# Performance work log

Hardware: AMD Instinct MI355X
Metric: run time of the kernel (lower is better)

## Reference

```python
import jax, jax.numpy as jnp
import numpy as np

B, S, H, I = 4, 2048, 2048, 5504


def setup_inputs() -> dict:
    key = jax.random.key(0)
    k1, k2, k3, k4 = jax.random.split(key, 4)
    scale = 0.02
    return {
        "hidden_state": jax.random.normal(k1, (B, S, H), dtype=jnp.float32),
        "w_gate": jax.random.normal(k2, (I, H), dtype=jnp.float32) * scale,  # gate_proj.weight [out,in]
        "w_up": jax.random.normal(k3, (I, H), dtype=jnp.float32) * scale,    # up_proj.weight
        "w_down": jax.random.normal(k4, (H, I), dtype=jnp.float32) * scale,  # down_proj.weight
    }


def reference(hidden_state, w_gate, w_up, w_down):
    # SwiGLU: act(x W_g^T) * (x W_u^T)
    gate = jax.nn.silu(jnp.einsum("bsh,ih->bsi", hidden_state, w_gate))
    up = jnp.einsum("bsh,ih->bsi", hidden_state, w_up)
    intermediate = gate * up  # [B,S,I]

    # Neuron impacts. Original broadcasts (B,I,1)*(1,I,H) and sums over H;
    # algebraically identical to s[b,i] * ||w_up[i,:]||^2, which we use to
    # avoid materializing the [B,I,H] tensor. Same math, same result.
    s = jnp.sum(intermediate ** 2, axis=1)          # sum over seq dim -> [B,I]
    row_sq = jnp.sum(w_up ** 2, axis=-1)            # [I]
    impacts = jnp.sqrt(s * row_sq[None, :])          # [B,I]

    out = jnp.einsum("bsi,hi->bsh", intermediate, w_down)  # down_proj
    return out, impacts
```

## Files before the change

kernel.cpp:

```cpp
#include <hip/hip_runtime.h>
#include <stdint.h>
#include <stddef.h>

typedef __attribute__((ext_vector_type(8))) short short8;
typedef __attribute__((ext_vector_type(4))) float f32x4;
typedef unsigned short u16;

#define B_ 4
#define S_ 2048
#define H_ 2048
#define I_ 5504
#define M_ 8192

__device__ __forceinline__ u16 f2bf(float f) {
  uint32_t u = __float_as_uint(f);
  u += 0x7fff + ((u >> 16) & 1);
  return (u16)(u >> 16);
}

#define GLOAD_LDS16(src, dst)                                                            \
  __builtin_amdgcn_global_load_lds((const __attribute__((address_space(1))) void*)(src), \
                                   (__attribute__((address_space(3))) void*)(dst), 16, 0, 0)

__global__ __launch_bounds__(256) void cvt_f32_bf16(const float* __restrict__ in,
                                                    u16* __restrict__ out, int n4) {
  int i = blockIdx.x * 256 + threadIdx.x;
  if (i < n4) {
    float4 v = ((const float4*)in)[i];
    ushort4 o;
    o.x = f2bf(v.x); o.y = f2bf(v.y); o.z = f2bf(v.z); o.w = f2bf(v.w);
    ((ushort4*)out)[i] = o;
  }
}

__global__ __launch_bounds__(256) void cvt_wcat(const float* __restrict__ wg,
                                                const float* __restrict__ wu,
                                                u16* __restrict__ wcat) {
  const int i = blockIdx.x * 256 + threadIdx.x;
  const int f = i * 4;
  const int r = f >> 11;
  const int c = f & 2047;
  const int srcrow = (r >> 5) * 16 + (r & 15);
  const float* src = (((r >> 4) & 1) ? wu : wg) + (size_t)srcrow * 2048 + c;
  float4 v = *(const float4*)src;
  ushort4 o;
  o.x = f2bf(v.x); o.y = f2bf(v.y); o.z = f2bf(v.z); o.w = f2bf(v.w);
  *(ushort4*)(wcat + (size_t)r * 2048 + c) = o;
}

#define WAITLGK0 asm volatile("s_waitcnt lgkmcnt(0)" ::: "memory")
#define PH_BAR asm volatile("s_barrier" ::: "memory")

#define MM2(av, bx, by, N0, N1)                                                             \
  {                                                                                         \
    __builtin_amdgcn_s_setprio(1);                                                          \
    _Pragma("unroll") for (int m = 0; m < 8; ++m) {                                         \
      acc[m][N0] = __builtin_amdgcn_mfma_f32_16x16x32_bf16(av[m], bx, acc[m][N0], 0, 0, 0); \
      acc[m][N1] = __builtin_amdgcn_mfma_f32_16x16x32_bf16(av[m], by, acc[m][N1], 0, 0, 0); \
    }                                                                                       \
    __builtin_amdgcn_s_setprio(0);                                                          \
  }

template <int EPI>
__global__ __launch_bounds__(512, 1) void gemm8(const u16* __restrict__ A,
                                                const u16* __restrict__ Bm, const int K,
                                                const int NT, float* __restrict__ outf,
                                                u16* __restrict__ inter, float* __restrict__ s) {
  __shared__ __align__(16) char lds_raw[131072 + 512];

  const int nwg = gridDim.x;
  const int cpx = nwg >> 3;
  const int swz = (blockIdx.x & 7) * cpx + (blockIdx.x >> 3);
  const int mt = swz / NT;
  const int nt = swz % NT;

  const int tid = threadIdx.x;
  const int lane = tid & 63;
  const int wid = tid >> 6;
  const int wr = wid >> 2;
  const int wc = wid & 3;
  const int l15 = lane & 15;

  if (tid < 128) ((float*)(lds_raw + 131072))[tid] = 0.f;

  const int chunkx = (l15 >> 1) & 3;
  const int aoff = (wr * 128 + l15) * 64 + (((lane >> 4) ^ chunkx) << 4);
  const int boff = (wc * 64 + l15) * 64 + (((lane >> 4) ^ chunkx) << 4);

  const u16* Abase = A + (size_t)(mt * 256) * K;
  const u16* Bbase = Bm + (size_t)(nt * 256) * K;

  int goff[2], loff[2];
#pragma unroll
  for (int i = 0; i < 2; ++i) {
    const int f = tid * 16 + i * 8192;
    const int row = f >> 6;
    const int cl = (f >> 4) & 3;
    goff[i] = row * K + 8 * (cl ^ ((row >> 1) & 3));
    loff[i] = (tid >> 6) * 1024 + i * 8192;
  }

#define STG(v, q)                                                              \
  {                                                                            \
    const u16* _b = ((q) < 2 ? Abase : Bbase) + (v) * 64 + ((q) & 1) * 32;     \
    char* _s = lds_raw + (((v) & 1) * 65536 + (q) * 16384);                    \
    GLOAD_LDS16(_b + goff[0], _s + loff[0]);                                   \
    GLOAD_LDS16(_b + goff[1], _s + loff[1]);                                   \
  }
#define RDA8(dst, c, ks)                                 \
  _Pragma("unroll") for (int m = 0; m < 8; ++m) dst[m] = \
      *(const short8*)(lds_raw + (c) * 65536 + (ks) * 16384 + aoff + m * 1024);
#define RDB(dst, c, ks, n) \
  dst = *(const short8*)(lds_raw + (c) * 65536 + 32768 + (ks) * 16384 + boff + (n) * 1024);

  f32x4 acc[8][4] = {};
  short8 a[8], a2[8];

  const int T = K >> 6;

  STG(0, 0); STG(0, 1); STG(0, 2); STG(0, 3);
  STG(1, 0); STG(1, 2); STG(1, 1);
  asm volatile("s_waitcnt vmcnt(6)" ::: "memory");
  PH_BAR;

#pragma unroll 1
  for (int t = 0; t < T; ++t) {
    const int c = t & 1;
    const bool s1 = (t + 1 < T);
    const bool s2 = (t + 2 < T);
    short8 b0x, b0y, b1x, b1y, b2x, b2y, b3x, b3y;
    RDA8(a, c, 0);
    RDB(b0x, c, 0, 0);
    RDB(b0y, c, 0, 1);
    if (s1) STG(t + 1, 3);
    WAITLGK0;
    PH_BAR;
    MM2(a, b0x, b0y, 0, 1);
    RDB(b1x, c, 0, 2);
    RDB(b1y, c, 0, 3);
    if (s2) STG(t + 2, 0);
    WAITLGK0;
    PH_BAR;
    MM2(a, b1x, b1y, 2, 3);
    RDA8(a2, c, 1);
    RDB(b2x, c, 1, 0);
    RDB(b2y, c, 1, 1);
    if (s2) STG(t + 2, 2);
    WAITLGK0;
    PH_BAR;
    MM2(a2, b2x, b2y, 0, 1);
    RDB(b3x, c, 1, 2);
    RDB(b3y, c, 1, 3);
    if (s2) STG(t + 2, 1);
    if (s2) {
      asm volatile("s_waitcnt vmcnt(6) lgkmcnt(0)" ::: "memory");
    } else {
      asm volatile("s_waitcnt vmcnt(0) lgkmcnt(0)" ::: "memory");
    }
    PH_BAR;
    MM2(a2, b3x, b3y, 2, 3);
  }

  const int r0 = mt * 256 + wr * 128 + (lane >> 4) * 4;
  if constexpr (EPI == 0) {
    const int c0 = nt * 256 + wc * 64 + l15;
#pragma unroll
    for (int m = 0; m < 8; ++m)
#pragma unroll
      for (int n = 0; n < 4; ++n)
#pragma unroll
        for (int j = 0; j < 4; ++j)
          outf[(size_t)(r0 + m * 16 + j) * 2048 + (c0 + n * 16)] = acc[m][n][j];
  } else {
    float* s_tile = (float*)(lds_raw + 131072);
    const int c0 = nt * 128 + wc * 32 + l15;
    float sp0 = 0.f, sp1 = 0.f;
#pragma unroll
    for (int m = 0; m < 8; ++m) {
#pragma unroll
      for (int j = 0; j < 4; ++j) {
        {
          const float g = acc[m][0][j], u = acc[m][1][j];
          const float v = (g / (1.f + __expf(-g))) * u;
          sp0 += v * v;
          inter[(size_t)(r0 + m * 16 + j) * I_ + c0] = f2bf(v);
        }
        {
          const float g = acc[m][2][j], u = acc[m][3][j];
          const float v = (g / (1.f + __expf(-g))) * u;
          sp1 += v * v;
          inter[(size_t)(r0 + m * 16 + j) * I_ + (c0 + 16)] = f2bf(v);
        }
      }
    }
    atomicAdd(&s_tile[wc * 32 + l15], sp0);
    atomicAdd(&s_tile[wc * 32 + 16 + l15], sp1);
    __syncthreads();
    if (tid < 128) atomicAdd(&s[(mt >> 3) * I_ + nt * 128 + tid], s_tile[tid]);
  }
#undef STG
#undef RDA8
#undef RDB
}

__global__ __launch_bounds__(256) void rowsq_impacts(const float* __restrict__ wu,
                                                     const float* __restrict__ s,
                                                     float* __restrict__ imp) {
  const int i = blockIdx.x;
  const int tid = threadIdx.x;
  const float4* row = (const float4*)(wu + (size_t)i * H_);
  float acc = 0.f;
#pragma unroll
  for (int t = 0; t < 2; ++t) {
    float4 v = row[tid + t * 256];
    acc += v.x * v.x + v.y * v.y + v.z * v.z + v.w * v.w;
  }
#pragma unroll
  for (int off = 32; off > 0; off >>= 1) acc += __shfl_down(acc, off, 64);
  __shared__ float wsum[4];
  if ((tid & 63) == 0) wsum[tid >> 6] = acc;
  __syncthreads();
  if (tid == 0) {
    const float rs = wsum[0] + wsum[1] + wsum[2] + wsum[3];
#pragma unroll
    for (int b = 0; b < 4; ++b) imp[b * I_ + i] = sqrtf(s[b * I_ + i] * rs);
  }
}

extern "C" void kernel_launch(void* const* d_in, const int* in_sizes, int n_in,
                              void* d_out, int out_size, void* d_ws, size_t ws_size,
                              hipStream_t stream) {
  const float* x = (const float*)d_in[0];
  const float* wg = (const float*)d_in[1];
  const float* wu = (const float*)d_in[2];
  const float* wd = (const float*)d_in[3];
  float* out = (float*)d_out;
  float* imp = out + (size_t)M_ * H_;

  char* ws = (char*)d_ws;
  u16* xb = (u16*)(ws);
  u16* wcatb = (u16*)(ws + 33554432);
  u16* wdb = (u16*)(ws + 78643200);
  u16* interb = (u16*)(ws + 101187584);
  float* s = (float*)(ws + 191365120);

  cvt_f32_bf16<<<16384, 256, 0, stream>>>(x, xb, (M_ * H_) / 4);
  cvt_wcat<<<22016, 256, 0, stream>>>(wg, wu, wcatb);
  cvt_f32_bf16<<<11008, 256, 0, stream>>>(wd, wdb, (H_ * I_) / 4);
  hipMemsetAsync(s, 0, (size_t)B_ * I_ * sizeof(float), stream);

  gemm8<1><<<1376, 512, 0, stream>>>(xb, wcatb, 2048, 43, nullptr, interb, s);
  gemm8<0><<<256, 512, 0, stream>>>(interb, wdb, 5504, 8, out, nullptr, nullptr);
  rowsq_impacts<<<I_, 256, 0, stream>>>(wu, s, imp);
}
```

Measured before the change: 713.2 us.

## Restructure GEMM main loop into quadrant-based MFMA phases with reused fragments

```diff
diff --git a/kernel.cpp b/kernel.cpp
--- a/kernel.cpp
+++ b/kernel.cpp
@@ -51,14 +51,16 @@
 #define WAITLGK0 asm volatile("s_waitcnt lgkmcnt(0)" ::: "memory")
 #define PH_BAR asm volatile("s_barrier" ::: "memory")
 
-#define MM2(av, bx, by, N0, N1)                                                             \
-  {                                                                                         \
-    __builtin_amdgcn_s_setprio(1);                                                          \
-    _Pragma("unroll") for (int m = 0; m < 8; ++m) {                                         \
-      acc[m][N0] = __builtin_amdgcn_mfma_f32_16x16x32_bf16(av[m], bx, acc[m][N0], 0, 0, 0); \
-      acc[m][N1] = __builtin_amdgcn_mfma_f32_16x16x32_bf16(av[m], by, acc[m][N1], 0, 0, 0); \
-    }                                                                                       \
-    __builtin_amdgcn_s_setprio(0);                                                          \
+#define MMQ(AF, BF, MB, N0)                                                              \
+  {                                                                                      \
+    __builtin_amdgcn_s_setprio(1);                                                       \
+    _Pragma("unroll") for (int m = 0; m < 4; ++m) _Pragma("unroll") for (int n = 0; n < 2; ++n) { \
+      acc[MB + m][N0 + n] =                                                              \
+          __builtin_amdgcn_mfma_f32_16x16x32_bf16(AF[0][m], BF[0][n], acc[MB + m][N0 + n], 0, 0, 0); \
+      acc[MB + m][N0 + n] =                                                              \
+          __builtin_amdgcn_mfma_f32_16x16x32_bf16(AF[1][m], BF[1][n], acc[MB + m][N0 + n], 0, 0, 0); \
+    }                                                                                    \
+    __builtin_amdgcn_s_setprio(0);                                                       \
   }
 
 template <int EPI>
@@ -100,27 +102,29 @@
     loff[i] = (tid >> 6) * 1024 + i * 8192;
   }
 
-#define STG(v, q)                                                              \
-  {                                                                            \
-    const u16* _b = ((q) < 2 ? Abase : Bbase) + (v) * 64 + ((q) & 1) * 32;     \
-    char* _s = lds_raw + (((v) & 1) * 65536 + (q) * 16384);                    \
-    GLOAD_LDS16(_b + goff[0], _s + loff[0]);                                   \
-    GLOAD_LDS16(_b + goff[1], _s + loff[1]);                                   \
-  }
-#define RDA8(dst, c, ks)                                 \
-  _Pragma("unroll") for (int m = 0; m < 8; ++m) dst[m] = \
-      *(const short8*)(lds_raw + (c) * 65536 + (ks) * 16384 + aoff + m * 1024);
-#define RDB(dst, c, ks, n) \
-  dst = *(const short8*)(lds_raw + (c) * 65536 + 32768 + (ks) * 16384 + boff + (n) * 1024);
+#define STG(v, q)                                                          \
+  {                                                                        \
+    const u16* _b = ((q) < 2 ? Abase : Bbase) + (v) * 64 + ((q) & 1) * 32; \
+    char* _s = lds_raw + (((v) & 1) * 65536 + (q) * 16384);                \
+    GLOAD_LDS16(_b + goff[0], _s + loff[0]);                               \
+    GLOAD_LDS16(_b + goff[1], _s + loff[1]);                               \
+  }
+#define RDAQ(dst, c, MB)                                                              \
+  _Pragma("unroll") for (int ks = 0; ks < 2; ++ks) _Pragma("unroll") for (int m = 0; m < 4; ++m) \
+      dst[ks][m] = *(const short8*)(lds_raw + (c) * 65536 + ks * 16384 + aoff + (MB + m) * 1024);
+#define RDBQ(dst, c, NB)                                                              \
+  _Pragma("unroll") for (int ks = 0; ks < 2; ++ks) _Pragma("unroll") for (int n = 0; n < 2; ++n) \
+      dst[ks][n] =                                                                    \
+          *(const short8*)(lds_raw + (c) * 65536 + 32768 + ks * 16384 + boff + (NB + n) * 1024);
 
   f32x4 acc[8][4] = {};
-  short8 a[8], a2[8];
+  short8 alo[2][4], ahi[2][4], b01[2][2], b23[2][2];
 
   const int T = K >> 6;
 
   STG(0, 0); STG(0, 1); STG(0, 2); STG(0, 3);
-  STG(1, 0); STG(1, 2); STG(1, 1);
-  asm volatile("s_waitcnt vmcnt(6)" ::: "memory");
+  STG(1, 2); STG(1, 3);
+  asm volatile("s_waitcnt vmcnt(4)" ::: "memory");
   PH_BAR;
 
 #pragma unroll 1
@@ -128,37 +132,34 @@
     const int c = t & 1;
     const bool s1 = (t + 1 < T);
     const bool s2 = (t + 2 < T);
-    short8 b0x, b0y, b1x, b1y, b2x, b2y, b3x, b3y;
-    RDA8(a, c, 0);
-    RDB(b0x, c, 0, 0);
-    RDB(b0y, c, 0, 1);
-    if (s1) STG(t + 1, 3);
+    RDAQ(alo, c, 0);
+    RDBQ(b01, c, 0);
+    if (s1) STG(t + 1, 0);
+    PH_BAR;
     WAITLGK0;
-    PH_BAR;
-    MM2(a, b0x, b0y, 0, 1);
-    RDB(b1x, c, 0, 2);
-    RDB(b1y, c, 0, 3);
-    if (s2) STG(t + 2, 0);
+    MMQ(alo, b01, 0, 0);
+    PH_BAR;
+    RDBQ(b23, c, 2);
+    if (s1) STG(t + 1, 1);
+    PH_BAR;
     WAITLGK0;
-    PH_BAR;
-    MM2(a, b1x, b1y, 2, 3);
-    RDA8(a2, c, 1);
-    RDB(b2x, c, 1, 0);
-    RDB(b2y, c, 1, 1);
+    MMQ(alo, b23, 0, 2);
+    PH_BAR;
+    RDAQ(ahi, c, 4);
     if (s2) STG(t + 2, 2);
+    PH_BAR;
     WAITLGK0;
-    PH_BAR;
-    MM2(a2, b2x, b2y, 0, 1);
-    RDB(b3x, c, 1, 2);
-    RDB(b3y, c, 1, 3);
-    if (s2) STG(t + 2, 1);
+    MMQ(ahi, b23, 4, 2);
+    PH_BAR;
+    if (s2) STG(t + 2, 3);
+    PH_BAR;
     if (s2) {
-      asm volatile("s_waitcnt vmcnt(6) lgkmcnt(0)" ::: "memory");
+      asm volatile("s_waitcnt vmcnt(4)" ::: "memory");
     } else {
-      asm volatile("s_waitcnt vmcnt(0) lgkmcnt(0)" ::: "memory");
+      asm volatile("s_waitcnt vmcnt(0)" ::: "memory");
     }
-    PH_BAR;
-    MM2(a2, b3x, b3y, 2, 3);
+    MMQ(ahi, b01, 4, 0);
+    PH_BAR;
   }
 
   const int r0 = mt * 256 + wr * 128 + (lane >> 4) * 4;
@@ -199,8 +200,8 @@
     if (tid < 128) atomicAdd(&s[(mt >> 3) * I_ + nt * 128 + tid], s_tile[tid]);
   }
 #undef STG
-#undef RDA8
-#undef RDB
+#undef RDAQ
+#undef RDBQ
 }
 
 __global__ __launch_bounds__(256) void rowsq_impacts(const float* __restrict__ wu,
```

New measurement: 739.9 us. +3.7%, slower.
